# Kernel tuning notes

Hardware: AMD Instinct MI355X
Metric: run time of the kernel (lower is better)

The kernel has to match this reference:

```python
import jax, jax.numpy as jnp
import numpy as np

B, T, E, H, L, V = 2, 1024, 1024, 16, 4, 32000
HS = E // H
EPS = 1e-5


def layernorm(x, g, b):
    m = jnp.mean(x, axis=-1, keepdims=True)
    v = jnp.mean((x - m) ** 2, axis=-1, keepdims=True)
    return (x - m) * jax.lax.rsqrt(v + EPS) * g + b


def setup_inputs() -> dict:
    key = jax.random.key(0)
    ks = jax.random.split(key, 20)
    s = 0.02
    inp = {
        "ids": jax.random.randint(ks[0], (B, T), 0, V, dtype=jnp.int32),
        "emb": jax.random.normal(ks[1], (V, E), jnp.float32) * s,
        "pos": jax.random.normal(ks[2], (T, E), jnp.float32) * s,
        "wq": jax.random.normal(ks[3], (L, E, E), jnp.float32) * s,
        "bq": jnp.zeros((L, E), jnp.float32),
        "wk": jax.random.normal(ks[4], (L, E, E), jnp.float32) * s,
        "bk": jnp.zeros((L, E), jnp.float32),
        "wv": jax.random.normal(ks[5], (L, E, E), jnp.float32) * s,
        "bv": jnp.zeros((L, E), jnp.float32),
        "w1": jax.random.normal(ks[6], (L, E, 4 * E), jnp.float32) * s,
        "b1": jnp.zeros((L, 4 * E), jnp.float32),
        "w2": jax.random.normal(ks[7], (L, 4 * E, E), jnp.float32) * s,
        "b2": jnp.zeros((L, E), jnp.float32),
        "ln1_g": jnp.ones((L, E), jnp.float32),
        "ln1_b": jnp.zeros((L, E), jnp.float32),
        "ln2_g": jnp.ones((L, E), jnp.float32),
        "ln2_b": jnp.zeros((L, E), jnp.float32),
        "proj_w": jax.random.normal(ks[8], (E, V), jnp.float32) * s,
        "proj_b": jnp.zeros((V,), jnp.float32),
    }
    return inp


def reference(ids, emb, pos, wq, bq, wk, bk, wv, bv, w1, b1, w2, b2,
              ln1_g, ln1_b, ln2_g, ln2_b, proj_w, proj_b):
    x = emb[ids] + pos[:ids.shape[-1]]  # [B,T,E]
    scale = 1.0 / (E ** 0.5)  # NOTE: original divides by embed_size**0.5
    causal = jnp.tril(jnp.ones((T, T), dtype=bool))
    for l in range(L):
        h = layernorm(x, ln1_g[l], ln1_b[l])
        q = (h @ wq[l] + bq[l]).reshape(B, T, H, HS).transpose(0, 2, 1, 3)
        k = (h @ wk[l] + bk[l]).reshape(B, T, H, HS).transpose(0, 2, 1, 3)
        v = (h @ wv[l] + bv[l]).reshape(B, T, H, HS).transpose(0, 2, 1, 3)
        scores = jnp.einsum('bhqd,bhkd->bhqk', q, k) * scale
        scores = jnp.where(causal, scores, -jnp.inf)
        attn = jax.nn.softmax(scores, axis=-1)
        o = jnp.einsum('bhqk,bhkd->bhqd', attn, v)
        o = o.transpose(0, 2, 1, 3).reshape(B, T, E)
        x = x + o
        h2 = layernorm(x, ln2_g[l], ln2_b[l])
        ff = jax.nn.gelu(h2 @ w1[l] + b1[l], approximate=False) @ w2[l] + b2[l]
        x = x + ff  # Dropout(0.2) in eval mode = identity
    logits = x @ proj_w + proj_b  # [B,T,V]
    return logits
```

## Files before the change

### kernel.cpp

```cpp
#include <hip/hip_runtime.h>
#include <hip/hip_bf16.h>
#include <cstdint>

#define B_    2
#define T_    1024
#define E_    1024
#define H_    16
#define HS_   64
#define L_    4
#define V_    32000
#define FF_   4096
#define BT_   2048
#define EPS_  1e-5f
#define SCALE_ 0.03125f

typedef __bf16 bf16;
typedef bf16  bf16x4 __attribute__((ext_vector_type(4)));
typedef bf16  bf16x8 __attribute__((ext_vector_type(8)));
typedef float f32x4  __attribute__((ext_vector_type(4)));

#define GL2LDS(gp, lp) __builtin_amdgcn_global_load_lds( \
    (const __attribute__((address_space(1))) void*)(gp), \
    (__attribute__((address_space(3))) void*)(lp), 16, 0, 0)

__global__ __launch_bounds__(256) void embed_kernel(
    const int* __restrict__ ids, const float* __restrict__ emb,
    const float* __restrict__ pos, float* __restrict__ x)
{
  int bt = blockIdx.x;
  int t  = bt & (T_ - 1);
  int id = ids[bt];
  f32x4 e = *(const f32x4*)(emb + (size_t)id * E_ + threadIdx.x * 4);
  f32x4 p = *(const f32x4*)(pos + (size_t)t  * E_ + threadIdx.x * 4);
  *(f32x4*)(x + (size_t)bt * E_ + threadIdx.x * 4) = e + p;
}

__device__ __forceinline__ float wred_sum(float v) {
#pragma unroll
  for (int o = 32; o; o >>= 1) v += __shfl_xor(v, o, 64);
  return v;
}

__global__ __launch_bounds__(256) void ln_kernel(
    const float* __restrict__ x, const float* __restrict__ g,
    const float* __restrict__ b, bf16* __restrict__ h)
{
  int row = blockIdx.x, tid = threadIdx.x;
  f32x4 v = *(const f32x4*)(x + (size_t)row * E_ + tid * 4);
  float s  = v[0] + v[1] + v[2] + v[3];
  float sq = v[0]*v[0] + v[1]*v[1] + v[2]*v[2] + v[3]*v[3];
  s  = wred_sum(s);
  sq = wred_sum(sq);
  __shared__ float rs[4], rq[4];
  int w = tid >> 6, lane = tid & 63;
  if (lane == 0) { rs[w] = s; rq[w] = sq; }
  __syncthreads();
  float S = rs[0] + rs[1] + rs[2] + rs[3];
  float Q = rq[0] + rq[1] + rq[2] + rq[3];
  float mean = S * (1.0f / E_);
  float var  = Q * (1.0f / E_) - mean * mean;
  float rstd = rsqrtf(fmaxf(var, 0.0f) + EPS_);
  f32x4 gv = *(const f32x4*)(g + tid * 4);
  f32x4 bv = *(const f32x4*)(b + tid * 4);
  f32x4 o = (v - mean) * rstd * gv + bv;
  bf16x4 ob = { (bf16)o[0], (bf16)o[1], (bf16)o[2], (bf16)o[3] };
  *(bf16x4*)(h + (size_t)row * E_ + tid * 4) = ob;
}

__global__ __launch_bounds__(256) void convw_kernel(
    const float* __restrict__ W0, const float* __restrict__ W1, const float* __restrict__ W2,
    bf16* __restrict__ O0, bf16* __restrict__ O1, bf16* __restrict__ O2,
    int K, int ldW)
{
  int z = blockIdx.z;
  const float* W = (z == 0) ? W0 : (z == 1) ? W1 : W2;
  bf16*        O = (z == 0) ? O0 : (z == 1) ? O1 : O2;
  __shared__ float tl[32][33];
  int n0 = blockIdx.x * 32, k0 = blockIdx.y * 32;
  int c = threadIdx.x & 31, r = threadIdx.x >> 5;
#pragma unroll
  for (int p = 0; p < 4; ++p)
    tl[r + p * 8][c] = W[(size_t)(k0 + r + p * 8) * ldW + n0 + c];
  __syncthreads();
#pragma unroll
  for (int p = 0; p < 4; ++p)
    O[(size_t)(n0 + r + p * 8) * K + k0 + c] = (bf16)tl[c][r + p * 8];
}

template <int ACT, int MODE>
__global__ __launch_bounds__(256) void gemm_bf16(
    const bf16* __restrict__ A,
    const bf16* __restrict__ B0, const bf16* __restrict__ B1, const bf16* __restrict__ B2,
    const float* __restrict__ bi0, const float* __restrict__ bi1, const float* __restrict__ bi2,
    bf16* __restrict__ Cb0, bf16* __restrict__ Cb1, bf16* __restrict__ Cb2,
    float* __restrict__ Cf, const float* __restrict__ R,
    int K, int ldc)
{
  int z = blockIdx.z;
  const bf16*  Bm = (z == 0) ? B0 : (z == 1) ? B1 : B2;
  const float* bi = (z == 0) ? bi0 : (z == 1) ? bi1 : bi2;
  bf16*        Cb = (z == 0) ? Cb0 : (z == 1) ? Cb1 : Cb2;

  int nb  = (int)(gridDim.x * gridDim.y);
  int lin = blockIdx.x + gridDim.x * blockIdx.y;
  int per = nb >> 3;
  int b   = (lin & 7) * per + (lin >> 3);
  int mi  = b & 15;
  int ni  = b >> 4;

  __shared__ __align__(16) char lds[2][16384];

  int tid = threadIdx.x;
  int lane = tid & 63, wid = tid >> 6;
  int wm = (wid >> 1) * 64, wn = (wid & 1) * 64;
  int fr = lane & 15, fb = lane >> 4;

  const bf16* Asrc = A  + (size_t)(mi * 128) * K;
  const bf16* Bsrc = Bm + (size_t)(ni * 128) * K;

  int NT = K >> 5;

#define STAGE(buf, kk)                                                          \
  {                                                                             \
    _Pragma("unroll")                                                           \
    for (int is = 0; is < 2; ++is) {                                            \
      int rl = is * 64 + (tid >> 2);                                            \
      int key = (rl >> 1) & 3;                                                  \
      int ck  = ((tid & 3) ^ key) * 8;                                          \
      GL2LDS(Asrc + (size_t)rl * K + (kk) + ck,                                 \
             lds[buf] + is * 4096 + tid * 16);                                  \
      GL2LDS(Bsrc + (size_t)rl * K + (kk) + ck,                                 \
             lds[buf] + 8192 + is * 4096 + tid * 16);                           \
    }                                                                           \
  }

  f32x4 acc[4][4];
#pragma unroll
  for (int i = 0; i < 4; ++i)
#pragma unroll
    for (int j = 0; j < 4; ++j) acc[i][j] = (f32x4){0.f, 0.f, 0.f, 0.f};

  STAGE(0, 0);
  int cur = 0;

  for (int t = 0; t < NT; ++t) {
    __syncthreads();
    if (t + 1 < NT) STAGE(cur ^ 1, (t + 1) << 5);

    const char* Ab = lds[cur];
    const char* Bb = lds[cur] + 8192;
    bf16x8 af[4], bfr[4];
#pragma unroll
    for (int i = 0; i < 4; ++i) {
      int rl = wm + i * 16 + fr;
      af[i] = *(const bf16x8*)(Ab + rl * 64 + ((fb ^ ((rl >> 1) & 3)) * 16));
    }
#pragma unroll
    for (int j = 0; j < 4; ++j) {
      int rl = wn + j * 16 + fr;
      bfr[j] = *(const bf16x8*)(Bb + rl * 64 + ((fb ^ ((rl >> 1) & 3)) * 16));
    }
#pragma unroll
    for (int i = 0; i < 4; ++i)
#pragma unroll
      for (int j = 0; j < 4; ++j)
        acc[i][j] = __builtin_amdgcn_mfma_f32_16x16x32_bf16(af[i], bfr[j], acc[i][j], 0, 0, 0);
    cur ^= 1;
  }
#undef STAGE

#pragma unroll
  for (int i = 0; i < 4; ++i) {
#pragma unroll
    for (int j = 0; j < 4; ++j) {
      int gc = ni * 128 + wn + j * 16 + fr;
      float bv = bi[gc];
#pragma unroll
      for (int r = 0; r < 4; ++r) {
        int gr = mi * 128 + wm + i * 16 + fb * 4 + r;
        float vv = acc[i][j][r] + bv;
        if (ACT == 1) vv = 0.5f * vv * (1.0f + erff(vv * 0.70710678118654752f));
        if (MODE == 2) {
          float nv = vv + R[(size_t)gr * ldc + gc];
          Cf[(size_t)gr * ldc + gc] = nv;
          Cb[(size_t)gr * ldc + gc] = (bf16)nv;
        } else if (MODE == 1) {
          Cb[(size_t)gr * ldc + gc] = (bf16)vv;
        } else {
          Cf[(size_t)gr * ldc + gc] = vv;
        }
      }
    }
  }
}

__global__ __launch_bounds__(256) void attn_kernel(
    const bf16* __restrict__ q, const bf16* __restrict__ k,
    const bf16* __restrict__ v, float* __restrict__ x)
{
  __shared__ __align__(16) char Ks[8192];
  __shared__ __align__(16) char Vs[8192];
  __shared__ __align__(16) char Ps[8192];

  int tid = threadIdx.x, lane = tid & 63, w = tid >> 6;
  int qt = blockIdx.x, bh = blockIdx.y;
  int b = bh >> 4, h = bh & 15;
  size_t hoff = (size_t)b * T_ * E_ + h * HS_;
  int fr = lane & 15, fb = lane >> 4;

  bf16x8 qa[2];
  {
    const bf16* qp = q + hoff + (size_t)(qt * 64 + w * 16 + fr) * E_ + fb * 8;
    qa[0] = *(const bf16x8*)qp;
    qa[1] = *(const bf16x8*)(qp + 32);
  }

  f32x4 O[4];
  float m_[4], l_[4];
#pragma unroll
  for (int i = 0; i < 4; ++i) { O[i] = (f32x4){0.f,0.f,0.f,0.f}; m_[i] = -1e30f; l_[i] = 0.f; }

  for (int kt = 0; kt <= qt; ++kt) {
    __syncthreads();
    {
      const bf16* kbase = k + hoff + (size_t)(kt * 64) * E_;
#pragma unroll
      for (int is = 0; is < 2; ++is) {
        int c = is * 32 + (tid >> 3);
        int key = ((c & 7) ^ (c >> 3)) & 7;
        GL2LDS(kbase + (size_t)c * E_ + (((tid & 7) ^ key) * 8),
               Ks + is * 4096 + tid * 16);
      }
    }
#pragma unroll
    for (int p = 0; p < 2; ++p) {
      int row = tid >> 2;
      int d0 = (tid & 3) * 8 + p * 32;
      bf16x8 vv = *(const bf16x8*)(v + hoff + (size_t)(kt * 64 + row) * E_ + d0);
#pragma unroll
      for (int e = 0; e < 8; ++e) {
        int d = d0 + e;
        int key = ((d & 7) ^ (d >> 3)) & 7;
        *(bf16*)(Vs + d * 128 + ((row * 2) ^ (key << 4))) = vv[e];
      }
    }
    __syncthreads();

    f32x4 s[4];
#pragma unroll
    for (int jc = 0; jc < 4; ++jc) {
      s[jc] = (f32x4){0.f, 0.f, 0.f, 0.f};
#pragma unroll
      for (int kc = 0; kc < 2; ++kc) {
        int c = jc * 16 + fr;
        int key = ((c & 7) ^ (c >> 3)) & 7;
        bf16x8 kf = *(const bf16x8*)(Ks + c * 128 + ((kc * 64 + fb * 16) ^ (key << 4)));
        s[jc] = __builtin_amdgcn_mfma_f32_16x16x32_bf16(qa[kc], kf, s[jc], 0, 0, 0);
      }
    }

    char* pbase = Ps + w * 2048;
#pragma unroll
    for (int r = 0; r < 4; ++r) {
      float s0 = s[0][r] * SCALE_, s1 = s[1][r] * SCALE_;
      float s2 = s[2][r] * SCALE_, s3 = s[3][r] * SCALE_;
      int qrow = qt * 64 + w * 16 + fb * 4 + r;
      if (kt == qt) {
        int kc0 = kt * 64 + fr;
        if (kc0      > qrow) s0 = -1e30f;
        if (kc0 + 16 > qrow) s1 = -1e30f;
        if (kc0 + 32 > qrow) s2 = -1e30f;
        if (kc0 + 48 > qrow) s3 = -1e30f;
      }
      float mx = fmaxf(fmaxf(s0, s1), fmaxf(s2, s3));
      mx = fmaxf(mx, __shfl_xor(mx, 1, 16));
      mx = fmaxf(mx, __shfl_xor(mx, 2, 16));
      mx = fmaxf(mx, __shfl_xor(mx, 4, 16));
      mx = fmaxf(mx, __shfl_xor(mx, 8, 16));
      float mnew = fmaxf(m_[r], mx);
      float p0 = __expf(s0 - mnew), p1 = __expf(s1 - mnew);
      float p2 = __expf(s2 - mnew), p3 = __expf(s3 - mnew);
      float rs = p0 + p1 + p2 + p3;
      rs += __shfl_xor(rs, 1, 16);
      rs += __shfl_xor(rs, 2, 16);
      rs += __shfl_xor(rs, 4, 16);
      rs += __shfl_xor(rs, 8, 16);
      float scl = __expf(m_[r] - mnew);
      l_[r] = l_[r] * scl + rs;
      m_[r] = mnew;
#pragma unroll
      for (int jd = 0; jd < 4; ++jd) O[jd][r] *= scl;
      int key2 = (r << 4) ^ (fb << 5);
      char* pr_ = pbase + (fb * 4 + r) * 128;
      *(bf16*)(pr_ + (( 0 + fr * 2) ^ key2)) = (bf16)p0;
      *(bf16*)(pr_ + ((32 + fr * 2) ^ key2)) = (bf16)p1;
      *(bf16*)(pr_ + ((64 + fr * 2) ^ key2)) = (bf16)p2;
      *(bf16*)(pr_ + ((96 + fr * 2) ^ key2)) = (bf16)p3;
    }

#pragma unroll
    for (int kc = 0; kc < 2; ++kc) {
      int key2 = ((fr & 3) << 4) ^ ((fr >> 2) << 5);
      bf16x8 pa = *(const bf16x8*)(pbase + fr * 128 + ((kc * 64 + fb * 16) ^ key2));
#pragma unroll
      for (int jd = 0; jd < 4; ++jd) {
        int d = jd * 16 + fr;
        int key = ((d & 7) ^ (d >> 3)) & 7;
        bf16x8 vf = *(const bf16x8*)(Vs + d * 128 + ((kc * 64 + fb * 16) ^ (key << 4)));
        O[jd] = __builtin_amdgcn_mfma_f32_16x16x32_bf16(pa, vf, O[jd], 0, 0, 0);
      }
    }
  }

#pragma unroll
  for (int r = 0; r < 4; ++r) {
    float inv = 1.0f / l_[r];
    float* xp = x + hoff + (size_t)(qt * 64 + w * 16 + fb * 4 + r) * E_;
#pragma unroll
    for (int jd = 0; jd < 4; ++jd) {
      int d = jd * 16 + fr;
      xp[d] += O[jd][r] * inv;
    }
  }
}

extern "C" void kernel_launch(void* const* d_in, const int* in_sizes, int n_in,
                              void* d_out, int out_size, void* d_ws, size_t ws_size,
                              hipStream_t stream)
{
  const int*   ids  = (const int*)  d_in[0];
  const float* emb  = (const float*)d_in[1];
  const float* pos  = (const float*)d_in[2];
  const float* wq   = (const float*)d_in[3];
  const float* bq   = (const float*)d_in[4];
  const float* wk   = (const float*)d_in[5];
  const float* bk   = (const float*)d_in[6];
  const float* wv   = (const float*)d_in[7];
  const float* bv   = (const float*)d_in[8];
  const float* w1   = (const float*)d_in[9];
  const float* b1   = (const float*)d_in[10];
  const float* w2   = (const float*)d_in[11];
  const float* b2   = (const float*)d_in[12];
  const float* ln1g = (const float*)d_in[13];
  const float* ln1b = (const float*)d_in[14];
  const float* ln2g = (const float*)d_in[15];
  const float* ln2b = (const float*)d_in[16];
  const float* pw   = (const float*)d_in[17];
  const float* pb   = (const float*)d_in[18];
  float* out = (float*)d_out;

  if (ws_size < (size_t)66 * 1024 * 1024) return;
  float* ws = (float*)d_ws;
  float* x   = ws;
  bf16*  xb  = (bf16*)(ws + (size_t) 2 * 1024 * 1024);
  bf16*  hb  = (bf16*)(ws + (size_t) 3 * 1024 * 1024);
  bf16*  qb  = (bf16*)(ws + (size_t) 4 * 1024 * 1024);
  bf16*  kb  = (bf16*)(ws + (size_t) 5 * 1024 * 1024);
  bf16*  vb  = (bf16*)(ws + (size_t) 6 * 1024 * 1024);
  bf16*  ffb = (bf16*)(ws + (size_t) 7 * 1024 * 1024);
  bf16*  lwb = (bf16*)(ws + (size_t)11 * 1024 * 1024);
  bf16*  pwb = (bf16*)(ws + (size_t) 3 * 1024 * 1024);
  bf16*  wqt = lwb;
  bf16*  wkt = lwb + (size_t)1 * 1024 * 1024;
  bf16*  wvt = lwb + (size_t)2 * 1024 * 1024;
  bf16*  w1t = lwb + (size_t)3 * 1024 * 1024;
  bf16*  w2t = lwb + (size_t)7 * 1024 * 1024;

  embed_kernel<<<BT_, 256, 0, stream>>>(ids, emb, pos, x);

  for (int l = 0; l < L_; ++l) {
    const size_t lEE = (size_t)l * E_ * E_;
    const size_t lEF = (size_t)l * E_ * FF_;

    convw_kernel<<<dim3(E_/32, E_/32, 3), 256, 0, stream>>>(
        wq + lEE, wk + lEE, wv + lEE, wqt, wkt, wvt, E_, E_);
    convw_kernel<<<dim3(FF_/32, E_/32, 1), 256, 0, stream>>>(
        w1 + lEF, nullptr, nullptr, w1t, nullptr, nullptr, E_, FF_);
    convw_kernel<<<dim3(E_/32, FF_/32, 1), 256, 0, stream>>>(
        w2 + lEF, nullptr, nullptr, w2t, nullptr, nullptr, FF_, E_);

    ln_kernel<<<BT_, 256, 0, stream>>>(x, ln1g + l*E_, ln1b + l*E_, hb);

    gemm_bf16<0,1><<<dim3(16, E_/128, 3), 256, 0, stream>>>(
        hb, wqt, wkt, wvt, bq + l*E_, bk + l*E_, bv + l*E_,
        qb, kb, vb, nullptr, nullptr, E_, E_);

    attn_kernel<<<dim3(T_/64, B_*H_), 256, 0, stream>>>(qb, kb, vb, x);

    ln_kernel<<<BT_, 256, 0, stream>>>(x, ln2g + l*E_, ln2b + l*E_, hb);

    gemm_bf16<1,1><<<dim3(16, FF_/128, 1), 256, 0, stream>>>(
        hb, w1t, nullptr, nullptr, b1 + (size_t)l*FF_, nullptr, nullptr,
        ffb, nullptr, nullptr, nullptr, nullptr, E_, FF_);

    gemm_bf16<0,2><<<dim3(16, E_/128, 1), 256, 0, stream>>>(
        ffb, w2t, nullptr, nullptr, b2 + l*E_, nullptr, nullptr,
        xb, nullptr, nullptr, x, x, FF_, E_);
  }

  for (int cchunk = 0; cchunk < 2; ++cchunk) {
    int c0 = cchunk * 16000;
    convw_kernel<<<dim3(16000/32, E_/32, 1), 256, 0, stream>>>(
        pw + c0, nullptr, nullptr, pwb, nullptr, nullptr, E_, V_);
    gemm_bf16<0,0><<<dim3(16, 16000/128, 1), 256, 0, stream>>>(
        xb, pwb, nullptr, nullptr, pb + c0, nullptr, nullptr,
        nullptr, nullptr, nullptr, out + c0, nullptr, E_, V_);
  }
}
```

Baseline: 954.7 us.

## Split-K the FFN down-projection and use a 256x256-tile GEMM for logits

The FFN down-projection GEMM is split into two K halves along grid z. This doubles the number of blocks for a small output. The two fp32 partials are summed, with bias and residual added, in a new combine kernel that also writes the bf16 copy of x. The vocabulary projection now converts the whole projection weight once. It then runs a new 512-thread GEMM with 256x256 tiles, 64-wide K stages, explicit vmcnt waits and MFMA priority raising, aiming for more reuse per byte loaded. Workspace buffers are rearranged so the transposed projection weight can overlay dead buffers, at the cost of a larger 128KB LDS footprint per block and extra partial-sum traffic.

```diff
diff --git a/kernel.cpp b/kernel.cpp
--- a/kernel.cpp
+++ b/kernel.cpp
@@ -94,12 +94,13 @@
     const float* __restrict__ bi0, const float* __restrict__ bi1, const float* __restrict__ bi2,
     bf16* __restrict__ Cb0, bf16* __restrict__ Cb1, bf16* __restrict__ Cb2,
     float* __restrict__ Cf, const float* __restrict__ R,
-    int K, int ldc)
+    int K, int ldc, int LDK)
 {
   int z = blockIdx.z;
-  const bf16*  Bm = (z == 0) ? B0 : (z == 1) ? B1 : B2;
+  const bf16*  Bm = (MODE == 3) ? B0 : (z == 0) ? B0 : (z == 1) ? B1 : B2;
   const float* bi = (z == 0) ? bi0 : (z == 1) ? bi1 : bi2;
   bf16*        Cb = (z == 0) ? Cb0 : (z == 1) ? Cb1 : Cb2;
+  int koff = (MODE == 3) ? z * K : 0;
 
   int nb  = (int)(gridDim.x * gridDim.y);
   int lin = blockIdx.x + gridDim.x * blockIdx.y;
@@ -115,8 +116,8 @@
   int wm = (wid >> 1) * 64, wn = (wid & 1) * 64;
   int fr = lane & 15, fb = lane >> 4;
 
-  const bf16* Asrc = A  + (size_t)(mi * 128) * K;
-  const bf16* Bsrc = Bm + (size_t)(ni * 128) * K;
+  const bf16* Asrc = A  + (size_t)(mi * 128) * LDK + koff;
+  const bf16* Bsrc = Bm + (size_t)(ni * 128) * LDK + koff;
 
   int NT = K >> 5;
 
@@ -127,9 +128,9 @@
       int rl = is * 64 + (tid >> 2);                                            \
       int key = (rl >> 1) & 3;                                                  \
       int ck  = ((tid & 3) ^ key) * 8;                                          \
-      GL2LDS(Asrc + (size_t)rl * K + (kk) + ck,                                 \
+      GL2LDS(Asrc + (size_t)rl * LDK + (kk) + ck,                               \
              lds[buf] + is * 4096 + tid * 16);                                  \
-      GL2LDS(Bsrc + (size_t)rl * K + (kk) + ck,                                 \
+      GL2LDS(Bsrc + (size_t)rl * LDK + (kk) + ck,                               \
              lds[buf] + 8192 + is * 4096 + tid * 16);                           \
     }                                                                           \
   }
@@ -174,7 +175,7 @@
 #pragma unroll
     for (int j = 0; j < 4; ++j) {
       int gc = ni * 128 + wn + j * 16 + fr;
-      float bv = bi[gc];
+      float bv = (MODE == 3) ? 0.f : bi[gc];
 #pragma unroll
       for (int r = 0; r < 4; ++r) {
         int gr = mi * 128 + wm + i * 16 + fb * 4 + r;
@@ -186,9 +187,135 @@
           Cb[(size_t)gr * ldc + gc] = (bf16)nv;
         } else if (MODE == 1) {
           Cb[(size_t)gr * ldc + gc] = (bf16)vv;
-        } else {
-          Cf[(size_t)gr * ldc + gc] = vv;
+        } else if (MODE == 3) {
+          Cf[(size_t)(z * BT_ + gr) * ldc + gc] = vv;
         }
+      }
+    }
+  }
+}
+
+__global__ __launch_bounds__(256) void combine_kernel(
+    const float* __restrict__ p, const float* __restrict__ bi,
+    float* __restrict__ x, bf16* __restrict__ xb)
+{
+  int row = blockIdx.x, tid = threadIdx.x;
+  size_t off = (size_t)row * E_ + tid * 4;
+  f32x4 a = *(const f32x4*)(p + off);
+  f32x4 c = *(const f32x4*)(p + (size_t)BT_ * E_ + off);
+  f32x4 bv = *(const f32x4*)(bi + tid * 4);
+  f32x4 xv = *(const f32x4*)(x + off);
+  f32x4 nv = xv + a + c + bv;
+  *(f32x4*)(x + off) = nv;
+  bf16x4 ob = { (bf16)nv[0], (bf16)nv[1], (bf16)nv[2], (bf16)nv[3] };
+  *(bf16x4*)(xb + off) = ob;
+}
+
+__global__ __launch_bounds__(512, 2) void gemm256_kernel(
+    const bf16* __restrict__ A, const bf16* __restrict__ Bm,
+    const float* __restrict__ bi, float* __restrict__ C, int K, int N)
+{
+  int nwg = (int)gridDim.x;
+  int per = nwg >> 3;
+  int bid = (int)blockIdx.x;
+  int tl  = (bid & 7) * per + (bid >> 3);
+  int mi  = tl & 7, ni = tl >> 3;
+
+  __shared__ __align__(16) char lds[2][65536];
+
+  int tid = threadIdx.x;
+  int lane = tid & 63, wid = tid >> 6;
+  int wr = wid >> 2, wc = wid & 3;
+  int fr = lane & 15, fb = lane >> 4;
+
+  const bf16* Asrc = A  + (size_t)(mi * 256) * K;
+  const bf16* Bsrc = Bm + (size_t)(ni * 256) * K;
+
+  int NT = K >> 6;
+
+#define STAGE256(buf, kk)                                                  \
+  { _Pragma("unroll")                                                      \
+    for (int h = 0; h < 2; ++h) {                                          \
+      _Pragma("unroll")                                                    \
+      for (int is = 0; is < 2; ++is) {                                     \
+        int ri  = is * 64 + (tid >> 3);                                    \
+        int ck  = (tid & 7) ^ (ri & 7);                                    \
+        int row = h * 128 + ri;                                            \
+        GL2LDS(Asrc + (size_t)row * K + (kk) + ck * 8,                     \
+               lds[buf] + h * 16384 + is * 8192 + tid * 16);               \
+        GL2LDS(Bsrc + (size_t)row * K + (kk) + ck * 8,                     \
+               lds[buf] + 32768 + h * 16384 + is * 8192 + tid * 16);       \
+      }                                                                    \
+    } }
+
+  f32x4 acc[8][4];
+#pragma unroll
+  for (int i = 0; i < 8; ++i)
+#pragma unroll
+    for (int j = 0; j < 4; ++j) acc[i][j] = (f32x4){0.f, 0.f, 0.f, 0.f};
+
+  STAGE256(0, 0);
+
+  for (int t = 0; t < NT; ++t) {
+    int buf = t & 1;
+    if (t + 1 < NT) {
+      STAGE256(buf ^ 1, (t + 1) << 6);
+      asm volatile("s_waitcnt vmcnt(8)" ::: "memory");
+    } else {
+      asm volatile("s_waitcnt vmcnt(0)" ::: "memory");
+    }
+    __builtin_amdgcn_s_barrier();
+    asm volatile("" ::: "memory");
+
+    const char* Ab = lds[buf];
+    const char* Bb = lds[buf] + 32768;
+
+    bf16x8 bfr[4][2];
+#pragma unroll
+    for (int n2 = 0; n2 < 4; ++n2) {
+      int row = wc * 64 + n2 * 16 + fr;
+#pragma unroll
+      for (int ks = 0; ks < 2; ++ks)
+        bfr[n2][ks] = *(const bf16x8*)(Bb + (row >> 7) * 16384 + (row & 127) * 128
+                                          + ((((ks * 4 + fb) ^ (fr & 7))) << 4));
+    }
+#pragma unroll
+    for (int q = 0; q < 4; ++q) {
+      bf16x8 af[2][2];
+#pragma unroll
+      for (int m2 = 0; m2 < 2; ++m2) {
+        int ri = (q * 2 + m2) * 16 + fr;
+#pragma unroll
+        for (int ks = 0; ks < 2; ++ks)
+          af[m2][ks] = *(const bf16x8*)(Ab + wr * 16384 + ri * 128
+                                           + ((((ks * 4 + fb) ^ (fr & 7))) << 4));
+      }
+      __builtin_amdgcn_s_setprio(1);
+#pragma unroll
+      for (int m2 = 0; m2 < 2; ++m2)
+#pragma unroll
+        for (int n2 = 0; n2 < 4; ++n2)
+#pragma unroll
+          for (int ks = 0; ks < 2; ++ks)
+            acc[q * 2 + m2][n2] = __builtin_amdgcn_mfma_f32_16x16x32_bf16(
+                af[m2][ks], bfr[n2][ks], acc[q * 2 + m2][n2], 0, 0, 0);
+      __builtin_amdgcn_s_setprio(0);
+    }
+    asm volatile("" ::: "memory");
+    __builtin_amdgcn_s_barrier();
+  }
+#undef STAGE256
+
+#pragma unroll
+  for (int i = 0; i < 8; ++i) {
+#pragma unroll
+    for (int j = 0; j < 4; ++j) {
+      int gc = ni * 256 + wc * 64 + j * 16 + fr;
+      float bv = bi[gc];
+#pragma unroll
+      for (int r = 0; r < 4; ++r) {
+        int gr = mi * 256 + wr * 128 + i * 16 + fb * 4 + r;
+        C[(size_t)gr * N + gc] = acc[i][j][r] + bv;
       }
     }
   }
@@ -349,17 +476,18 @@
   const float* pb   = (const float*)d_in[18];
   float* out = (float*)d_out;
 
-  if (ws_size < (size_t)66 * 1024 * 1024) return;
+  if (ws_size < (size_t)17 * 1024 * 1024 * 4) return;
   float* ws = (float*)d_ws;
   float* x   = ws;
-  bf16*  xb  = (bf16*)(ws + (size_t) 2 * 1024 * 1024);
-  bf16*  hb  = (bf16*)(ws + (size_t) 3 * 1024 * 1024);
-  bf16*  qb  = (bf16*)(ws + (size_t) 4 * 1024 * 1024);
-  bf16*  kb  = (bf16*)(ws + (size_t) 5 * 1024 * 1024);
-  bf16*  vb  = (bf16*)(ws + (size_t) 6 * 1024 * 1024);
-  bf16*  ffb = (bf16*)(ws + (size_t) 7 * 1024 * 1024);
-  bf16*  lwb = (bf16*)(ws + (size_t)11 * 1024 * 1024);
-  bf16*  pwb = (bf16*)(ws + (size_t) 3 * 1024 * 1024);
+  bf16*  hb  = (bf16*)(ws + (size_t) 2 * 1024 * 1024);
+  bf16*  qb  = (bf16*)(ws + (size_t) 3 * 1024 * 1024);
+  bf16*  kb  = (bf16*)(ws + (size_t) 4 * 1024 * 1024);
+  bf16*  vb  = (bf16*)(ws + (size_t) 5 * 1024 * 1024);
+  bf16*  ffb = (bf16*)(ws + (size_t) 6 * 1024 * 1024);
+  float* fp  = ws + (size_t)2 * 1024 * 1024;
+  bf16*  lwb = (bf16*)(ws + (size_t)10 * 1024 * 1024);
+  bf16*  xb  = (bf16*)(ws + (size_t)16 * 1024 * 1024);
+  bf16*  pwb = (bf16*)ws;
   bf16*  wqt = lwb;
   bf16*  wkt = lwb + (size_t)1 * 1024 * 1024;
   bf16*  wvt = lwb + (size_t)2 * 1024 * 1024;
@@ -383,7 +511,7 @@
 
     gemm_bf16<0,1><<<dim3(16, E_/128, 3), 256, 0, stream>>>(
         hb, wqt, wkt, wvt, bq + l*E_, bk + l*E_, bv + l*E_,
-        qb, kb, vb, nullptr, nullptr, E_, E_);
+        qb, kb, vb, nullptr, nullptr, E_, E_, E_);
 
     attn_kernel<<<dim3(T_/64, B_*H_), 256, 0, stream>>>(qb, kb, vb, x);
 
@@ -391,19 +519,16 @@
 
     gemm_bf16<1,1><<<dim3(16, FF_/128, 1), 256, 0, stream>>>(
         hb, w1t, nullptr, nullptr, b1 + (size_t)l*FF_, nullptr, nullptr,
-        ffb, nullptr, nullptr, nullptr, nullptr, E_, FF_);
-
-    gemm_bf16<0,2><<<dim3(16, E_/128, 1), 256, 0, stream>>>(
-        ffb, w2t, nullptr, nullptr, b2 + l*E_, nullptr, nullptr,
-        xb, nullptr, nullptr, x, x, FF_, E_);
-  }
-
-  for (int cchunk = 0; cchunk < 2; ++cchunk) {
-    int c0 = cchunk * 16000;
-    convw_kernel<<<dim3(16000/32, E_/32, 1), 256, 0, stream>>>(
-        pw + c0, nullptr, nullptr, pwb, nullptr, nullptr, E_, V_);
-    gemm_bf16<0,0><<<dim3(16, 16000/128, 1), 256, 0, stream>>>(
-        xb, pwb, nullptr, nullptr, pb + c0, nullptr, nullptr,
-        nullptr, nullptr, nullptr, out + c0, nullptr, E_, V_);
-  }
-}
+        ffb, nullptr, nullptr, nullptr, nullptr, E_, FF_, E_);
+
+    gemm_bf16<0,3><<<dim3(16, E_/128, 2), 256, 0, stream>>>(
+        ffb, w2t, nullptr, nullptr, nullptr, nullptr, nullptr,
+        nullptr, nullptr, nullptr, fp, nullptr, FF_/2, E_, FF_);
+    combine_kernel<<<BT_, 256, 0, stream>>>(fp, b2 + l*E_, x, xb);
+  }
+
+  convw_kernel<<<dim3(V_/32, E_/32, 1), 256, 0, stream>>>(
+      pw, nullptr, nullptr, pwb, nullptr, nullptr, E_, V_);
+  gemm256_kernel<<<(V_/256) * 8, 512, 0, stream>>>(
+      xb, pwb, pb, out, E_, V_);
+}
```

Result: faster. 860.6 us (-9.9%).
